# Optimization experiments

Measured on AMD Instinct MI355X. Metric: run time of the kernel, lower is better.

## Reference

```python
import jax, jax.numpy as jnp
import numpy as np

B, S, H = 2, 4096, 2048
NH, HD = 16, 128
BLOCK = 256
EPS = 1e-5


def setup_inputs() -> dict:
    key = jax.random.key(0)
    ks = jax.random.split(key, 6)
    return {
        "hidden_states": jax.random.normal(ks[0], (B, S, H), jnp.float32),
        "attention_mask": jnp.ones((B, S), jnp.float32),
        "slope_rate": jax.random.uniform(ks[1], (NH,), jnp.float32),
        "w_qkv": jax.random.normal(ks[2], (H, 3 * NH * HD), jnp.float32) * 0.02,
        "w_gate": jax.random.normal(ks[3], (H, NH * HD), jnp.float32) * 0.02,
        "w_out": jax.random.normal(ks[4], (NH * HD, H), jnp.float32) * 0.02,
        "norm_weight": jnp.ones((NH * HD,), jnp.float32),
    }


def _lightning_attention(q, k, v, slope):
    # q,k,v: [b,h,n,d]; slope: [h] positive decay rates
    b, h, n, d = q.shape
    nc = n // BLOCK
    ar = jnp.arange(BLOCK, dtype=q.dtype) + 1.0  # 1..BLOCK
    s = slope[:, None, None]  # [h,1,1]
    q_decay = jnp.exp(-s * ar[None, :, None])             # [h,BLOCK,1]
    k_decay = jnp.exp(-s * (BLOCK - ar)[None, :, None])   # [h,BLOCK,1]
    idx = ar[:, None] - ar[None, :]                        # [BLOCK,BLOCK]
    mask = (idx >= 0).astype(q.dtype)
    # mask idx before exp so masked entries don't overflow (keeps grads finite)
    diag_decay = jnp.exp(-s * (idx * mask)[None]) * mask[None]  # [h,BLOCK,BLOCK]
    block_decay = jnp.exp(-slope * BLOCK)[None, :, None, None]  # [1,h,1,1]

    def to_chunks(x):
        return x.reshape(b, h, nc, BLOCK, d).transpose(2, 0, 1, 3, 4)

    qc, kc, vc = to_chunks(q), to_chunks(k), to_chunks(v)

    def step(kv, xs):
        qi, ki, vi = xs  # [b,h,BLOCK,d]
        # inter-chunk: decayed query against carried state kv [b,h,d,d]
        o_inter = jnp.einsum("bhmd,bhde->bhme", qi * q_decay, kv)
        # intra-chunk: causal decayed attention
        attn = jnp.einsum("bhmd,bhnd->bhmn", qi, ki) * diag_decay
        o = o_inter + jnp.einsum("bhmn,bhne->bhme", attn, vi)
        kv = block_decay * kv + jnp.einsum("bhnd,bhne->bhde", ki * k_decay, vi)
        return kv, o

    kv0 = jnp.zeros((b, h, d, d), q.dtype)
    _, o = jax.lax.scan(step, kv0, (qc, kc, vc))  # o: [nc,b,h,BLOCK,d]
    return o.transpose(1, 2, 0, 3, 4).reshape(b, h, n, d)


def reference(hidden_states, attention_mask, slope_rate, w_qkv, w_gate, w_out, norm_weight):
    b, n, _ = hidden_states.shape
    qkv = jax.nn.silu(hidden_states @ w_qkv)  # act on fused qkv
    q, k, v = jnp.split(qkv, 3, axis=-1)

    def heads(x):
        return x.reshape(b, n, NH, HD).transpose(0, 2, 1, 3)

    q, k, v = heads(q), heads(k), heads(v)
    v = v * attention_mask[:, None, :, None]  # zero padded tokens
    o = _lightning_attention(q, k, v, slope_rate)  # [b,h,n,d]
    o = o.transpose(0, 2, 1, 3).reshape(b, n, NH * HD)
    # RMSNorm over head_dim*num_heads
    var = jnp.mean(o * o, axis=-1, keepdims=True)
    o = o * jax.lax.rsqrt(var + EPS) * norm_weight
    # sigmoid output gate from raw hidden_states
    o = jax.nn.sigmoid(hidden_states @ w_gate) * o
    return o @ w_out
```

## Files before the change

kernel.cpp:

```cpp
#include <hip/hip_runtime.h>
#include <cstdint>

#define B_ 2
#define S_ 4096
#define H_ 2048
#define NH_ 16
#define HD_ 128
#define BLOCK_ 256
#define NC_ (S_/BLOCK_)
#define M_ (B_*S_)
#define EPS_ 1e-5f

typedef unsigned short ushort_t;
typedef unsigned short u16x4 __attribute__((ext_vector_type(4)));
typedef short frag_ab __attribute__((ext_vector_type(8)));
typedef float frag_cd __attribute__((ext_vector_type(4)));

static __device__ inline float bf2f(ushort_t u) {
    union { unsigned int i; float f; } x;
    x.i = ((unsigned int)u) << 16;
    return x.f;
}
static __device__ inline ushort_t f2bf(float f) {
    union { float f; unsigned int i; } x;
    x.f = f;
    unsigned int r = x.i + 0x7fffu + ((x.i >> 16) & 1u);
    return (ushort_t)(r >> 16);
}

static __device__ __forceinline__ void gload_lds16(const ushort_t* g, ushort_t* l) {
    __builtin_amdgcn_global_load_lds(
        (__attribute__((address_space(1))) void*)(uintptr_t)g,
        (__attribute__((address_space(3))) void*)l,
        16, 0, 0);
}

#define FENCE_ asm volatile("" ::: "memory")
#define VMW0_  asm volatile("s_waitcnt vmcnt(0)" ::: "memory")

__global__ __launch_bounds__(256)
void cast_bf16_kernel(const float* __restrict__ in, ushort_t* __restrict__ out)
{
    int i = blockIdx.x * 256 + threadIdx.x;
    float4 v = reinterpret_cast<const float4*>(in)[i];
    u16x4 o = { f2bf(v.x), f2bf(v.y), f2bf(v.z), f2bf(v.w) };
    *reinterpret_cast<u16x4*>(&out[(size_t)i * 4]) = o;
}

__global__ __launch_bounds__(256)
void transpose_cast_kernel(const float* __restrict__ W, ushort_t* __restrict__ WT,
                           int K, int N)
{
    __shared__ float t[32][33];
    const int kb = blockIdx.y * 32, nb = blockIdx.x * 32;
    const int tx = threadIdx.x & 31, ty = threadIdx.x >> 5;
    #pragma unroll
    for (int i = 0; i < 4; ++i)
        t[ty + i * 8][tx] = W[(size_t)(kb + ty + i * 8) * N + nb + tx];
    __syncthreads();
    #pragma unroll
    for (int i = 0; i < 4; ++i)
        WT[(size_t)(nb + ty + i * 8) * K + kb + tx] = f2bf(t[tx][ty + i * 8]);
}

template<int MODE>
__global__ __launch_bounds__(256, 2)
void gemm128(const ushort_t* __restrict__ A, const ushort_t* __restrict__ BT,
             int M, int N, int K,
             float* __restrict__ Cf,
             ushort_t* __restrict__ qo, ushort_t* __restrict__ ko,
             ushort_t* __restrict__ kTo, ushort_t* __restrict__ vTo,
             ushort_t* __restrict__ gateo, const float* __restrict__ mask)
{
    __shared__ __align__(16) ushort_t LA[2][8192];
    __shared__ __align__(16) ushort_t LB[2][8192];

    const int tid  = threadIdx.x;
    const int lane = tid & 63, wid = tid >> 6;
    const int wm = wid >> 1, wn = wid & 1;
    const int l15 = lane & 15, l4 = lane >> 4;
    const int trow = tid >> 3;
    const int xk   = (tid & 7) ^ (trow & 7);

    const int nwg = gridDim.x;
    const int lin = blockIdx.x;
    const int virt = (lin & 7) * (nwg >> 3) + (lin >> 3);
    const int NBX = N >> 7;
    const int by = virt / NBX, bx = virt - by * NBX;
    const int rowBase = by * 128, colBase = bx * 128;

    frag_cd acc[4][4];
    #pragma unroll
    for (int m = 0; m < 4; ++m)
        #pragma unroll
        for (int n = 0; n < 4; ++n) acc[m][n] = 0.f;

    frag_ab fa[4][2];
    frag_ab fb[4][2];

    #define RDF(Lp, row_, sl_) \
        (*reinterpret_cast<const frag_ab*>( \
            reinterpret_cast<const char*>(Lp) + (row_) * 128 + ((((sl_) ^ ((row_) & 7)) & 7) << 4)))
    #define STG(Gp, base_, i_, kt_, Lp) \
        gload_lds16((Gp) + (size_t)((base_) + (i_) * 32 + trow) * K + (kt_) + xk * 8, \
                    (Lp) + (i_) * 2048 + wid * 512)

    const int NT = K >> 6;
    int cur = 0;
    #pragma unroll
    for (int i = 0; i < 4; ++i) { STG(A, rowBase, i, 0, LA[0]); STG(BT, colBase, i, 0, LB[0]); }
    VMW0_; FENCE_; __builtin_amdgcn_s_barrier();
    __builtin_amdgcn_sched_barrier(0);

    for (int t = 0; t < NT; ++t) {
        const ushort_t* Ab = LA[cur];
        const ushort_t* Bb = LB[cur];
        ushort_t* An = LA[cur ^ 1];
        ushort_t* Bn = LB[cur ^ 1];
        const int ktn = (t + 1) << 6;
        const bool more = (t + 1) < NT;

        if (more) {
            #pragma unroll
            for (int i = 0; i < 4; ++i) { STG(A, rowBase, i, ktn, An); STG(BT, colBase, i, ktn, Bn); }
        }

        #pragma unroll
        for (int ni = 0; ni < 4; ++ni)
            #pragma unroll
            for (int ks = 0; ks < 2; ++ks)
                fb[ni][ks] = RDF(Bb, wn * 64 + ni * 16 + l15, ks * 4 + l4);
        #pragma unroll
        for (int mi = 0; mi < 4; ++mi)
            #pragma unroll
            for (int ks = 0; ks < 2; ++ks)
                fa[mi][ks] = RDF(Ab, wm * 64 + mi * 16 + l15, ks * 4 + l4);

        __builtin_amdgcn_s_setprio(1);
        #pragma unroll
        for (int mi = 0; mi < 4; ++mi)
            #pragma unroll
            for (int ni = 0; ni < 4; ++ni)
                #pragma unroll
                for (int ks = 0; ks < 2; ++ks)
                    acc[mi][ni] = __builtin_amdgcn_mfma_f32_16x16x32_bf16(
                        fa[mi][ks], fb[ni][ks], acc[mi][ni], 0, 0, 0);
        __builtin_amdgcn_s_setprio(0);

        VMW0_; FENCE_; __builtin_amdgcn_s_barrier();
        __builtin_amdgcn_sched_barrier(0);
        cur ^= 1;
    }
    #undef RDF
    #undef STG

    const int row0 = rowBase + wm * 64;
    const int c0   = colBase + wn * 64;
    if (MODE == 0) {
        #pragma unroll
        for (int m = 0; m < 4; ++m) {
            #pragma unroll
            for (int n = 0; n < 4; ++n) {
                #pragma unroll
                for (int r = 0; r < 4; ++r) {
                    int row = row0 + m * 16 + l4 * 4 + r;
                    int col = c0 + n * 16 + l15;
                    Cf[(size_t)row * N + col] = acc[m][n][r];
                }
            }
        }
    } else {
        const int which = c0 >> 11;
        const int h     = (c0 >> 7) & 15;
        const int d0    = c0 & 127;
        const int b     = row0 >> 12;
        const int bh    = b * NH_ + h;
        #pragma unroll
        for (int m = 0; m < 4; ++m) {
            int sr0 = (row0 & 4095) + m * 16 + l4 * 4;
            #pragma unroll
            for (int n = 0; n < 4; ++n) {
                float x0 = acc[m][n][0], x1 = acc[m][n][1];
                float x2 = acc[m][n][2], x3 = acc[m][n][3];
                if (which == 3) {
                    int col_g = (c0 - 6144) + n * 16 + l15;
                    ushort_t* gp = gateo + (size_t)(row0 + m * 16 + l4 * 4) * H_ + col_g;
                    gp[0]       = f2bf(1.f / (1.f + __expf(-x0)));
                    gp[H_]      = f2bf(1.f / (1.f + __expf(-x1)));
                    gp[2 * H_]  = f2bf(1.f / (1.f + __expf(-x2)));
                    gp[3 * H_]  = f2bf(1.f / (1.f + __expf(-x3)));
                } else {
                    int d = d0 + n * 16 + l15;
                    float s0 = x0 / (1.f + __expf(-x0));
                    float s1 = x1 / (1.f + __expf(-x1));
                    float s2 = x2 / (1.f + __expf(-x2));
                    float s3 = x3 / (1.f + __expf(-x3));
                    if (which == 0) {
                        ushort_t* qp = qo + ((size_t)bh * S_ + sr0) * HD_ + d;
                        qp[0]        = f2bf(s0);
                        qp[HD_]      = f2bf(s1);
                        qp[2 * HD_]  = f2bf(s2);
                        qp[3 * HD_]  = f2bf(s3);
                    } else if (which == 1) {
                        u16x4 pk = { f2bf(s0), f2bf(s1), f2bf(s2), f2bf(s3) };
                        ushort_t* kp = ko + ((size_t)bh * S_ + sr0) * HD_ + d;
                        kp[0] = pk[0]; kp[HD_] = pk[1]; kp[2 * HD_] = pk[2]; kp[3 * HD_] = pk[3];
                        *reinterpret_cast<u16x4*>(&kTo[((size_t)bh * HD_ + d) * S_ + sr0]) = pk;
                    } else {
                        float mk0 = mask[b * S_ + sr0],     mk1 = mask[b * S_ + sr0 + 1];
                        float mk2 = mask[b * S_ + sr0 + 2], mk3 = mask[b * S_ + sr0 + 3];
                        u16x4 pk = { f2bf(s0 * mk0), f2bf(s1 * mk1), f2bf(s2 * mk2), f2bf(s3 * mk3) };
                        *reinterpret_cast<u16x4*>(&vTo[((size_t)bh * HD_ + d) * S_ + sr0]) = pk;
                    }
                }
            }
        }
    }
}

__global__ __launch_bounds__(256)
void kv_chunk_mfma(const ushort_t* __restrict__ kT, const ushort_t* __restrict__ vT,
                   const float* __restrict__ slope, ushort_t* __restrict__ kvT)
{
    const int c = blockIdx.x, bh = blockIdx.y;
    const float s = slope[bh & 15];
    const int tid = threadIdx.x, lane = tid & 63, w = tid >> 6;
    const int l15 = lane & 15, l4 = lane >> 4;
    __shared__ float dec[BLOCK_];
    __shared__ __align__(16) ushort_t VTl[128 * 64];
    __shared__ __align__(16) ushort_t KTl[128 * 64];
    dec[tid] = __expf(-s * (float)(BLOCK_ - 1 - tid));

    frag_cd acc[2][8];
    #pragma unroll
    for (int mf = 0; mf < 2; ++mf)
        #pragma unroll
        for (int df = 0; df < 8; ++df) acc[mf][df] = 0.f;

    for (int nt = 0; nt < 4; ++nt) {
        __syncthreads();
        #pragma unroll
        for (int i = 0; i < 4; ++i) {
            int u = tid + i * 256;
            int row = u >> 3, slot = u & 7;
            size_t gsrc = ((size_t)bh * HD_ + row) * S_ + c * BLOCK_ + nt * 64 + slot * 8;
            frag_ab v8 = *reinterpret_cast<const frag_ab*>(vT + gsrc);
            *reinterpret_cast<frag_ab*>((char*)VTl + row * 128 + ((slot * 16) ^ ((row & 7) << 4))) = v8;
            frag_ab k8 = *reinterpret_cast<const frag_ab*>(kT + gsrc);
            frag_ab kd;
            #pragma unroll
            for (int j = 0; j < 8; ++j)
                kd[j] = (short)f2bf(bf2f((ushort_t)k8[j]) * dec[nt * 64 + slot * 8 + j]);
            *reinterpret_cast<frag_ab*>((char*)KTl + row * 128 + ((slot * 16) ^ ((row & 7) << 4))) = kd;
        }
        __syncthreads();
        #pragma unroll
        for (int ks = 0; ks < 2; ++ks) {
            frag_ab a[2];
            #pragma unroll
            for (int mf = 0; mf < 2; ++mf)
                a[mf] = *reinterpret_cast<const frag_ab*>(
                    (char*)VTl + (w * 32 + mf * 16 + l15) * 128 + ((ks * 64 + l4 * 16) ^ ((l15 & 7) << 4)));
            #pragma unroll
            for (int df = 0; df < 8; ++df) {
                frag_ab bk = *reinterpret_cast<const frag_ab*>(
                    (char*)KTl + (df * 16 + l15) * 128 + ((ks * 64 + l4 * 16) ^ ((l15 & 7) << 4)));
                acc[0][df] = __builtin_amdgcn_mfma_f32_16x16x32_bf16(a[0], bk, acc[0][df], 0, 0, 0);
                acc[1][df] = __builtin_amdgcn_mfma_f32_16x16x32_bf16(a[1], bk, acc[1][df], 0, 0, 0);
            }
        }
    }
    ushort_t* out = kvT + ((size_t)bh * NC_ + c) * 16384;
    #pragma unroll
    for (int mf = 0; mf < 2; ++mf)
        #pragma unroll
        for (int df = 0; df < 8; ++df)
            #pragma unroll
            for (int r = 0; r < 4; ++r) {
                int e = w * 32 + mf * 16 + l4 * 4 + r;
                int d = df * 16 + l15;
                out[e * 128 + d] = f2bf(acc[mf][df][r]);
            }
}

__global__ __launch_bounds__(256)
void kv_scan_kernel(const float* __restrict__ slope, const ushort_t* __restrict__ kvT,
                    ushort_t* __restrict__ sT)
{
    const int es = blockIdx.x, bh = blockIdx.y;
    const float s = slope[bh & 15];
    const float bd = __expf(-s * (float)BLOCK_);
    const int tid = threadIdx.x;
    float st[16];
    #pragma unroll
    for (int i = 0; i < 16; ++i) st[i] = 0.f;
    for (int c = 0; c < NC_; ++c) {
        const ushort_t* p = kvT + ((size_t)bh * NC_ + c) * 16384;
        ushort_t* qp = sT + ((size_t)bh * NC_ + c) * 16384;
        #pragma unroll
        for (int i = 0; i < 16; ++i) {
            int lin = tid + i * 256;
            int off = (lin >> 5) * 128 + es * 32 + (lin & 31);
            float x = bf2f(p[off]);
            qp[off] = f2bf(st[i]);
            st[i] = bd * st[i] + x;
        }
    }
}

__global__ __launch_bounds__(512)
void attn_mfma(const ushort_t* __restrict__ q, const ushort_t* __restrict__ k,
               const ushort_t* __restrict__ vT, const ushort_t* __restrict__ sT,
               const float* __restrict__ slope, float* __restrict__ o)
{
    const int c = blockIdx.x, bh = blockIdx.y;
    const int h = bh & 15, b = bh >> 4;
    const float s = slope[h];
    const int tid = threadIdx.x, lane = tid & 63, w = tid >> 6;
    const int l15 = lane & 15, l4 = lane >> 4;

    __shared__ __align__(16) ushort_t SH[16384];
    __shared__ __align__(16) ushort_t P[8][2048];

    frag_ab aq[2][4];
    #pragma unroll
    for (int mf = 0; mf < 2; ++mf)
        #pragma unroll
        for (int ks = 0; ks < 4; ++ks) {
            int row = c * BLOCK_ + w * 32 + mf * 16 + l15;
            aq[mf][ks] = *reinterpret_cast<const frag_ab*>(
                q + ((size_t)bh * S_ + row) * HD_ + ks * 32 + l4 * 8);
        }

    frag_cd oa[2][8];
    #pragma unroll
    for (int mf = 0; mf < 2; ++mf)
        #pragma unroll
        for (int ef = 0; ef < 8; ++ef) oa[mf][ef] = 0.f;

    const int wrow = w * 32;
    for (int nt = 0; nt < 4; ++nt) {
        __syncthreads();
        #pragma unroll
        for (int i = 0; i < 2; ++i) {
            int u = tid + i * 512;
            int n = u >> 4, slot = u & 15;
            frag_ab k8 = *reinterpret_cast<const frag_ab*>(
                k + ((size_t)bh * S_ + c * BLOCK_ + nt * 64 + n) * HD_ + slot * 8);
            *reinterpret_cast<frag_ab*>((char*)SH + n * 256 + ((slot * 16) ^ ((n & 7) << 4))) = k8;
        }
        #pragma unroll
        for (int i = 0; i < 2; ++i) {
            int u = tid + i * 512;
            int e = u >> 3, slot = u & 7;
            frag_ab v8 = *reinterpret_cast<const frag_ab*>(
                vT + ((size_t)bh * HD_ + e) * S_ + c * BLOCK_ + nt * 64 + slot * 8);
            *reinterpret_cast<frag_ab*>((char*)SH + 16384 + e * 128 + ((slot * 16) ^ ((e & 7) << 4))) = v8;
        }
        __syncthreads();
        if (nt * 64 > wrow + 31) continue;

        frag_cd pacc[2][4];
        #pragma unroll
        for (int mf = 0; mf < 2; ++mf)
            #pragma unroll
            for (int nf = 0; nf < 4; ++nf) pacc[mf][nf] = 0.f;
        #pragma unroll
        for (int ks = 0; ks < 4; ++ks)
            #pragma unroll
            for (int nf = 0; nf < 4; ++nf) {
                frag_ab bk = *reinterpret_cast<const frag_ab*>(
                    (char*)SH + (nf * 16 + l15) * 256 + ((ks * 64 + l4 * 16) ^ ((l15 & 7) << 4)));
                pacc[0][nf] = __builtin_amdgcn_mfma_f32_16x16x32_bf16(aq[0][ks], bk, pacc[0][nf], 0, 0, 0);
                pacc[1][nf] = __builtin_amdgcn_mfma_f32_16x16x32_bf16(aq[1][ks], bk, pacc[1][nf], 0, 0, 0);
            }
        #pragma unroll
        for (int mf = 0; mf < 2; ++mf)
            #pragma unroll
            for (int nf = 0; nf < 4; ++nf)
                #pragma unroll
                for (int r = 0; r < 4; ++r) {
                    int m = mf * 16 + l4 * 4 + r;
                    int mrow = wrow + m;
                    int ncol = nt * 64 + nf * 16 + l15;
                    float pv = 0.f;
                    if (mrow >= ncol) pv = pacc[mf][nf][r] * __expf(s * (float)(ncol - mrow));
                    *reinterpret_cast<ushort_t*>(
                        (char*)&P[w][0] + m * 128 + (((nf * 16 + l15) * 2) ^ ((m & 7) << 4))) = f2bf(pv);
                }
        __builtin_amdgcn_sched_barrier(0);
        #pragma unroll
        for (int ks = 0; ks < 2; ++ks) {
            frag_ab ap[2];
            #pragma unroll
            for (int mf = 0; mf < 2; ++mf)
                ap[mf] = *reinterpret_cast<const frag_ab*>(
                    (char*)&P[w][0] + (mf * 16 + l15) * 128 + ((ks * 64 + l4 * 16) ^ ((l15 & 7) << 4)));
            #pragma unroll
            for (int ef = 0; ef < 8; ++ef) {
                frag_ab bv = *reinterpret_cast<const frag_ab*>(
                    (char*)SH + 16384 + (ef * 16 + l15) * 128 + ((ks * 64 + l4 * 16) ^ ((l15 & 7) << 4)));
                oa[0][ef] = __builtin_amdgcn_mfma_f32_16x16x32_bf16(ap[0], bv, oa[0][ef], 0, 0, 0);
                oa[1][ef] = __builtin_amdgcn_mfma_f32_16x16x32_bf16(ap[1], bv, oa[1][ef], 0, 0, 0);
            }
        }
    }

    __syncthreads();
    #pragma unroll
    for (int i = 0; i < 4; ++i) {
        int u = tid + i * 512;
        int e = u >> 4, slot = u & 15;
        frag_ab s8 = *reinterpret_cast<const frag_ab*>(
            sT + ((size_t)(bh * NC_ + c)) * 16384 + e * 128 + slot * 8);
        *reinterpret_cast<frag_ab*>((char*)SH + e * 256 + ((slot * 16) ^ ((e & 7) << 4))) = s8;
    }
    __syncthreads();
    #pragma unroll
    for (int mf = 0; mf < 2; ++mf) {
        float qd = __expf(-s * (float)(wrow + mf * 16 + l15 + 1));
        #pragma unroll
        for (int ks = 0; ks < 4; ++ks) {
            frag_ab v = aq[mf][ks];
            #pragma unroll
            for (int j = 0; j < 8; ++j)
                v[j] = (short)f2bf(bf2f((ushort_t)v[j]) * qd);
            aq[mf][ks] = v;
        }
    }
    #pragma unroll
    for (int ks = 0; ks < 4; ++ks)
        #pragma unroll
        for (int ef = 0; ef < 8; ++ef) {
            frag_ab bs = *reinterpret_cast<const frag_ab*>(
                (char*)SH + (ef * 16 + l15) * 256 + ((ks * 64 + l4 * 16) ^ ((l15 & 7) << 4)));
            oa[0][ef] = __builtin_amdgcn_mfma_f32_16x16x32_bf16(aq[0][ks], bs, oa[0][ef], 0, 0, 0);
            oa[1][ef] = __builtin_amdgcn_mfma_f32_16x16x32_bf16(aq[1][ks], bs, oa[1][ef], 0, 0, 0);
        }
    #pragma unroll
    for (int mf = 0; mf < 2; ++mf)
        #pragma unroll
        for (int ef = 0; ef < 8; ++ef)
            #pragma unroll
            for (int r = 0; r < 4; ++r) {
                int row = c * BLOCK_ + wrow + mf * 16 + l4 * 4 + r;
                int col = h * HD_ + ef * 16 + l15;
                o[((size_t)(b * S_ + row)) * H_ + col] = oa[mf][ef][r];
            }
}

__global__ __launch_bounds__(256)
void norm_gate_kernel(const float* __restrict__ o, const ushort_t* __restrict__ gate,
                      const float* __restrict__ nw, ushort_t* __restrict__ on)
{
    const int row = blockIdx.x;
    const int tid = threadIdx.x;
    const float* orow = o + (size_t)row * H_;
    const ushort_t* grow = gate + (size_t)row * H_;
    ushort_t* onrow = on + (size_t)row * H_;
    float vals[8];
    float ss = 0.f;
    #pragma unroll
    for (int i = 0; i < 8; ++i) {
        vals[i] = orow[tid + i * 256];
        ss += vals[i] * vals[i];
    }
    __shared__ float red[256];
    red[tid] = ss;
    __syncthreads();
    #pragma unroll
    for (int st = 128; st > 0; st >>= 1) {
        if (tid < st) red[tid] += red[tid + st];
        __syncthreads();
    }
    float scale = rsqrtf(red[0] * (1.f / (float)H_) + EPS_);
    #pragma unroll
    for (int i = 0; i < 8; ++i) {
        int cidx = tid + i * 256;
        onrow[cidx] = f2bf(vals[i] * scale * nw[cidx] * bf2f(grow[cidx]));
    }
}

extern "C" void kernel_launch(void* const* d_in, const int* in_sizes, int n_in,
                              void* d_out, int out_size, void* d_ws, size_t ws_size,
                              hipStream_t stream)
{
    const float* hidden = (const float*)d_in[0];
    const float* mask   = (const float*)d_in[1];
    const float* slope  = (const float*)d_in[2];
    const float* w_qkv  = (const float*)d_in[3];
    const float* w_gate = (const float*)d_in[4];
    const float* w_out  = (const float*)d_in[5];
    const float* nw     = (const float*)d_in[6];

    const size_t MH = (size_t)M_ * H_;
    ushort_t* hid_bf  = (ushort_t*)d_ws;
    ushort_t* on_ws   = hid_bf;
    ushort_t* wqkvT   = hid_bf + MH;
    ushort_t* wgateT  = wqkvT + (size_t)6144 * 2048;
    ushort_t* kvT_ws  = wqkvT;
    ushort_t* sT_ws   = wqkvT + MH / 2;
    ushort_t* woutT   = wqkvT;
    ushort_t* q_ws    = hid_bf + 2 * MH;
    ushort_t* k_ws    = q_ws + MH;
    ushort_t* vT_ws   = k_ws + MH;
    ushort_t* gate_ws = vT_ws + MH;
    ushort_t* kT_ws   = (ushort_t*)d_out;
    float*    o_f32   = (float*)d_out;

    dim3 blk(256);
    cast_bf16_kernel<<<(MH / 4) / 256, blk, 0, stream>>>(hidden, hid_bf);
    transpose_cast_kernel<<<dim3(6144 / 32, 2048 / 32), blk, 0, stream>>>(w_qkv, wqkvT, 2048, 6144);
    transpose_cast_kernel<<<dim3(2048 / 32, 2048 / 32), blk, 0, stream>>>(w_gate, wgateT, 2048, 2048);
    gemm128<2><<<dim3((M_ / 128) * (8192 / 128)), blk, 0, stream>>>(
        hid_bf, wqkvT, M_, 8192, 2048,
        nullptr, q_ws, k_ws, kT_ws, vT_ws, gate_ws, mask);
    kv_chunk_mfma<<<dim3(NC_, B_ * NH_), blk, 0, stream>>>(kT_ws, vT_ws, slope, kvT_ws);
    kv_scan_kernel<<<dim3(4, B_ * NH_), blk, 0, stream>>>(slope, kvT_ws, sT_ws);
    attn_mfma<<<dim3(NC_, B_ * NH_), dim3(512), 0, stream>>>(
        q_ws, k_ws, vT_ws, sT_ws, slope, o_f32);
    transpose_cast_kernel<<<dim3(2048 / 32, 2048 / 32), blk, 0, stream>>>(w_out, woutT, 2048, 2048);
    norm_gate_kernel<<<M_, blk, 0, stream>>>(o_f32, gate_ws, nw, on_ws);
    gemm128<0><<<dim3((M_ / 128) * (2048 / 128)), blk, 0, stream>>>(
        on_ws, woutT, M_, 2048, 2048,
        (float*)d_out, nullptr, nullptr, nullptr, nullptr, nullptr, nullptr);
}
```

Before: 591.8 us.

## Use 256x256 tile, 8-wave GEMM with interleaved prefetch for fused QKV/gate projection

Replaces the 128x128, 4-wave GEMM for the large QKV+gate projection with a 256x256 tile, 512-thread kernel. Each wave computes a 128x64 sub-tile. Global-to-LDS prefetches for the next K tile are split into chunks interleaved between MFMA groups, with partial vmcnt waits instead of a full drain. The aim is more data reuse per LDS load and better overlap of memory traffic with compute. The cost is 128KB of LDS per block, more accumulator registers, fewer blocks in the grid, and a delicate wait-count ordering that must stay correct. The output GEMM keeps the old 128 kernel, now specialised.

```diff
diff --git a/kernel.cpp b/kernel.cpp
--- a/kernel.cpp
+++ b/kernel.cpp
@@ -36,6 +36,8 @@
 }
 
 #define FENCE_ asm volatile("" ::: "memory")
+#define VMW8_  asm volatile("s_waitcnt vmcnt(8)" ::: "memory")
+#define VMW2_  asm volatile("s_waitcnt vmcnt(2)" ::: "memory")
 #define VMW0_  asm volatile("s_waitcnt vmcnt(0)" ::: "memory")
 
 __global__ __launch_bounds__(256)
@@ -64,20 +66,20 @@
 }
 
 template<int MODE>
-__global__ __launch_bounds__(256, 2)
-void gemm128(const ushort_t* __restrict__ A, const ushort_t* __restrict__ BT,
+__global__ __launch_bounds__(512, 2)
+void gemm256(const ushort_t* __restrict__ A, const ushort_t* __restrict__ BT,
              int M, int N, int K,
              float* __restrict__ Cf,
              ushort_t* __restrict__ qo, ushort_t* __restrict__ ko,
              ushort_t* __restrict__ kTo, ushort_t* __restrict__ vTo,
              ushort_t* __restrict__ gateo, const float* __restrict__ mask)
 {
-    __shared__ __align__(16) ushort_t LA[2][8192];
-    __shared__ __align__(16) ushort_t LB[2][8192];
+    __shared__ __align__(16) ushort_t LA[2][16384];
+    __shared__ __align__(16) ushort_t LB[2][16384];
 
     const int tid  = threadIdx.x;
     const int lane = tid & 63, wid = tid >> 6;
-    const int wm = wid >> 1, wn = wid & 1;
+    const int wm = wid >> 2, wn = wid & 3;
     const int l15 = lane & 15, l4 = lane >> 4;
     const int trow = tid >> 3;
     const int xk   = (tid & 7) ^ (trow & 7);
@@ -85,112 +87,152 @@
     const int nwg = gridDim.x;
     const int lin = blockIdx.x;
     const int virt = (lin & 7) * (nwg >> 3) + (lin >> 3);
-    const int NBX = N >> 7;
+    const int NBX = N >> 8;
     const int by = virt / NBX, bx = virt - by * NBX;
-    const int rowBase = by * 128, colBase = bx * 128;
-
-    frag_cd acc[4][4];
-    #pragma unroll
-    for (int m = 0; m < 4; ++m)
+    const int rowBase = by * 256, colBase = bx * 256;
+
+    frag_cd acc[8][4];
+    #pragma unroll
+    for (int m = 0; m < 8; ++m)
         #pragma unroll
         for (int n = 0; n < 4; ++n) acc[m][n] = 0.f;
 
     frag_ab fa[4][2];
-    frag_ab fb[4][2];
+    frag_ab fb[2][2][2];
 
     #define RDF(Lp, row_, sl_) \
         (*reinterpret_cast<const frag_ab*>( \
             reinterpret_cast<const char*>(Lp) + (row_) * 128 + ((((sl_) ^ ((row_) & 7)) & 7) << 4)))
     #define STG(Gp, base_, i_, kt_, Lp) \
-        gload_lds16((Gp) + (size_t)((base_) + (i_) * 32 + trow) * K + (kt_) + xk * 8, \
-                    (Lp) + (i_) * 2048 + wid * 512)
+        gload_lds16((Gp) + (size_t)((base_) + (i_) * 64 + trow) * K + (kt_) + xk * 8, \
+                    (Lp) + (i_) * 4096 + wid * 512)
 
     const int NT = K >> 6;
-    int cur = 0;
-    #pragma unroll
-    for (int i = 0; i < 4; ++i) { STG(A, rowBase, i, 0, LA[0]); STG(BT, colBase, i, 0, LB[0]); }
-    VMW0_; FENCE_; __builtin_amdgcn_s_barrier();
+
+    #define KTILE(AbP, BbP, AnP, BnP, TNEXT)                                        \
+    do {                                                                            \
+        const bool more = (TNEXT) < NT;                                             \
+        const int ktn = (TNEXT) << 6;                                               \
+                                                                            \
+        _Pragma("unroll")                                                           \
+        for (int mi = 0; mi < 4; ++mi)                                              \
+            _Pragma("unroll")                                                       \
+            for (int ks = 0; ks < 2; ++ks)                                          \
+                fa[mi][ks] = RDF(AbP, wm * 128 + mi * 16 + l15, ks * 4 + l4);       \
+        _Pragma("unroll")                                                           \
+        for (int ni = 0; ni < 2; ++ni)                                              \
+            _Pragma("unroll")                                                       \
+            for (int ks = 0; ks < 2; ++ks)                                          \
+                fb[0][ni][ks] = RDF(BbP, wn * 64 + ni * 16 + l15, ks * 4 + l4);     \
+        if (more) { STG(BT, colBase, 0, ktn, BnP); STG(BT, colBase, 1, ktn, BnP); } \
+        __builtin_amdgcn_s_setprio(1);                                              \
+        _Pragma("unroll")                                                           \
+        for (int mi = 0; mi < 4; ++mi)                                              \
+            _Pragma("unroll")                                                       \
+            for (int ni = 0; ni < 2; ++ni)                                          \
+                _Pragma("unroll")                                                   \
+                for (int ks = 0; ks < 2; ++ks)                                      \
+                    acc[mi][ni] = __builtin_amdgcn_mfma_f32_16x16x32_bf16(          \
+                        fa[mi][ks], fb[0][ni][ks], acc[mi][ni], 0, 0, 0);           \
+        __builtin_amdgcn_s_setprio(0);                                              \
+                                                                            \
+        _Pragma("unroll")                                                           \
+        for (int ni = 0; ni < 2; ++ni)                                              \
+            _Pragma("unroll")                                                       \
+            for (int ks = 0; ks < 2; ++ks)                                          \
+                fb[1][ni][ks] = RDF(BbP, wn * 64 + 32 + ni * 16 + l15, ks * 4 + l4);\
+        if (more) { STG(BT, colBase, 2, ktn, BnP); STG(BT, colBase, 3, ktn, BnP); } \
+        __builtin_amdgcn_s_setprio(1);                                              \
+        _Pragma("unroll")                                                           \
+        for (int mi = 0; mi < 4; ++mi)                                              \
+            _Pragma("unroll")                                                       \
+            for (int ni = 0; ni < 2; ++ni)                                          \
+                _Pragma("unroll")                                                   \
+                for (int ks = 0; ks < 2; ++ks)                                      \
+                    acc[mi][2 + ni] = __builtin_amdgcn_mfma_f32_16x16x32_bf16(      \
+                        fa[mi][ks], fb[1][ni][ks], acc[mi][2 + ni], 0, 0, 0);       \
+        __builtin_amdgcn_s_setprio(0);                                              \
+        if (more) { VMW8_; } else { VMW0_; }                                        \
+        FENCE_; __builtin_amdgcn_s_barrier();                                       \
+        __builtin_amdgcn_sched_barrier(0);                                          \
+                                                                            \
+        _Pragma("unroll")                                                           \
+        for (int mi = 0; mi < 4; ++mi)                                              \
+            _Pragma("unroll")                                                       \
+            for (int ks = 0; ks < 2; ++ks)                                          \
+                fa[mi][ks] = RDF(AbP, wm * 128 + 64 + mi * 16 + l15, ks * 4 + l4);  \
+        if (more) { STG(A, rowBase, 0, ktn, AnP); STG(A, rowBase, 2, ktn, AnP); }   \
+        __builtin_amdgcn_s_setprio(1);                                              \
+        _Pragma("unroll")                                                           \
+        for (int mi = 0; mi < 4; ++mi)                                              \
+            _Pragma("unroll")                                                       \
+            for (int ni = 0; ni < 2; ++ni)                                          \
+                _Pragma("unroll")                                                   \
+                for (int ks = 0; ks < 2; ++ks)                                      \
+                    acc[4 + mi][ni] = __builtin_amdgcn_mfma_f32_16x16x32_bf16(      \
+                        fa[mi][ks], fb[0][ni][ks], acc[4 + mi][ni], 0, 0, 0);       \
+        __builtin_amdgcn_s_setprio(0);                                              \
+                                                                            \
+        if (more) { STG(A, rowBase, 1, ktn, AnP); STG(A, rowBase, 3, ktn, AnP); }   \
+        __builtin_amdgcn_s_setprio(1);                                              \
+        _Pragma("unroll")                                                           \
+        for (int mi = 0; mi < 4; ++mi)                                              \
+            _Pragma("unroll")                                                       \
+            for (int ni = 0; ni < 2; ++ni)                                          \
+                _Pragma("unroll")                                                   \
+                for (int ks = 0; ks < 2; ++ks)                                      \
+                    acc[4 + mi][2 + ni] = __builtin_amdgcn_mfma_f32_16x16x32_bf16(  \
+                        fa[mi][ks], fb[1][ni][ks], acc[4 + mi][2 + ni], 0, 0, 0);   \
+        __builtin_amdgcn_s_setprio(0);                                              \
+        if (more) { VMW2_; }                                                        \
+        FENCE_; __builtin_amdgcn_s_barrier();                                       \
+        __builtin_amdgcn_sched_barrier(0);                                          \
+    } while (0)
+
+    STG(BT, colBase, 0, 0, &LB[0][0]); STG(BT, colBase, 1, 0, &LB[0][0]);
+    STG(BT, colBase, 2, 0, &LB[0][0]); STG(BT, colBase, 3, 0, &LB[0][0]);
+    STG(A,  rowBase, 0, 0, &LA[0][0]); STG(A,  rowBase, 2, 0, &LA[0][0]);
+    STG(A,  rowBase, 1, 0, &LA[0][0]); STG(A,  rowBase, 3, 0, &LA[0][0]);
+    VMW2_; FENCE_; __builtin_amdgcn_s_barrier();
     __builtin_amdgcn_sched_barrier(0);
 
-    for (int t = 0; t < NT; ++t) {
-        const ushort_t* Ab = LA[cur];
-        const ushort_t* Bb = LB[cur];
-        ushort_t* An = LA[cur ^ 1];
-        ushort_t* Bn = LB[cur ^ 1];
-        const int ktn = (t + 1) << 6;
-        const bool more = (t + 1) < NT;
-
-        if (more) {
-            #pragma unroll
-            for (int i = 0; i < 4; ++i) { STG(A, rowBase, i, ktn, An); STG(BT, colBase, i, ktn, Bn); }
-        }
-
-        #pragma unroll
-        for (int ni = 0; ni < 4; ++ni)
-            #pragma unroll
-            for (int ks = 0; ks < 2; ++ks)
-                fb[ni][ks] = RDF(Bb, wn * 64 + ni * 16 + l15, ks * 4 + l4);
-        #pragma unroll
-        for (int mi = 0; mi < 4; ++mi)
-            #pragma unroll
-            for (int ks = 0; ks < 2; ++ks)
-                fa[mi][ks] = RDF(Ab, wm * 64 + mi * 16 + l15, ks * 4 + l4);
-
-        __builtin_amdgcn_s_setprio(1);
-        #pragma unroll
-        for (int mi = 0; mi < 4; ++mi)
-            #pragma unroll
-            for (int ni = 0; ni < 4; ++ni)
-                #pragma unroll
-                for (int ks = 0; ks < 2; ++ks)
-                    acc[mi][ni] = __builtin_amdgcn_mfma_f32_16x16x32_bf16(
-                        fa[mi][ks], fb[ni][ks], acc[mi][ni], 0, 0, 0);
-        __builtin_amdgcn_s_setprio(0);
-
-        VMW0_; FENCE_; __builtin_amdgcn_s_barrier();
-        __builtin_amdgcn_sched_barrier(0);
-        cur ^= 1;
-    }
+    for (int t2 = 0; t2 < NT; t2 += 2) {
+        KTILE(&LA[0][0], &LB[0][0], &LA[1][0], &LB[1][0], t2 + 1);
+        KTILE(&LA[1][0], &LB[1][0], &LA[0][0], &LB[0][0], t2 + 2);
+    }
+    #undef KTILE
     #undef RDF
     #undef STG
 
-    const int row0 = rowBase + wm * 64;
+    const int row0 = rowBase + wm * 128;
     const int c0   = colBase + wn * 64;
-    if (MODE == 0) {
-        #pragma unroll
-        for (int m = 0; m < 4; ++m) {
-            #pragma unroll
-            for (int n = 0; n < 4; ++n) {
-                #pragma unroll
-                for (int r = 0; r < 4; ++r) {
-                    int row = row0 + m * 16 + l4 * 4 + r;
-                    int col = c0 + n * 16 + l15;
-                    Cf[(size_t)row * N + col] = acc[m][n][r];
-                }
-            }
-        }
-    } else {
+    {
         const int which = c0 >> 11;
         const int h     = (c0 >> 7) & 15;
         const int d0    = c0 & 127;
         const int b     = row0 >> 12;
         const int bh    = b * NH_ + h;
         #pragma unroll
-        for (int m = 0; m < 4; ++m) {
-            int sr0 = (row0 & 4095) + m * 16 + l4 * 4;
+        for (int m = 0; m < 8; ++m) {
+            int mr = (m >> 2) * 64 + (m & 3) * 16;
+            int sr0 = (row0 & 4095) + mr + l4 * 4;
             #pragma unroll
             for (int n = 0; n < 4; ++n) {
+                int nc = (n >> 1) * 32 + (n & 1) * 16;
                 float x0 = acc[m][n][0], x1 = acc[m][n][1];
                 float x2 = acc[m][n][2], x3 = acc[m][n][3];
-                if (which == 3) {
-                    int col_g = (c0 - 6144) + n * 16 + l15;
-                    ushort_t* gp = gateo + (size_t)(row0 + m * 16 + l4 * 4) * H_ + col_g;
+                if (MODE == 0) {
+                    float* cp = Cf + (size_t)(row0 + mr + l4 * 4) * N + c0 + nc + l15;
+                    cp[0] = x0; cp[N] = x1; cp[2 * (size_t)N] = x2; cp[3 * (size_t)N] = x3;
+                } else if (which == 3) {
+                    int col_g = (c0 - 6144) + nc + l15;
+                    ushort_t* gp = gateo + (size_t)(row0 + mr + l4 * 4) * H_ + col_g;
                     gp[0]       = f2bf(1.f / (1.f + __expf(-x0)));
                     gp[H_]      = f2bf(1.f / (1.f + __expf(-x1)));
                     gp[2 * H_]  = f2bf(1.f / (1.f + __expf(-x2)));
                     gp[3 * H_]  = f2bf(1.f / (1.f + __expf(-x3)));
                 } else {
-                    int d = d0 + n * 16 + l15;
+                    int d = d0 + nc + l15;
                     float s0 = x0 / (1.f + __expf(-x0));
                     float s1 = x1 / (1.f + __expf(-x1));
                     float s2 = x2 / (1.f + __expf(-x2));
@@ -218,6 +260,106 @@
     }
 }
 
+__global__ __launch_bounds__(256, 2)
+void gemm128(const ushort_t* __restrict__ A, const ushort_t* __restrict__ BT,
+             int M, int N, int K, float* __restrict__ Cf)
+{
+    __shared__ __align__(16) ushort_t LA[2][8192];
+    __shared__ __align__(16) ushort_t LB[2][8192];
+
+    const int tid  = threadIdx.x;
+    const int lane = tid & 63, wid = tid >> 6;
+    const int wm = wid >> 1, wn = wid & 1;
+    const int l15 = lane & 15, l4 = lane >> 4;
+    const int trow = tid >> 3;
+    const int xk   = (tid & 7) ^ (trow & 7);
+
+    const int nwg = gridDim.x;
+    const int lin = blockIdx.x;
+    const int virt = (lin & 7) * (nwg >> 3) + (lin >> 3);
+    const int NBX = N >> 7;
+    const int by = virt / NBX, bx = virt - by * NBX;
+    const int rowBase = by * 128, colBase = bx * 128;
+
+    frag_cd acc[4][4];
+    #pragma unroll
+    for (int m = 0; m < 4; ++m)
+        #pragma unroll
+        for (int n = 0; n < 4; ++n) acc[m][n] = 0.f;
+
+    frag_ab fa[4][2];
+    frag_ab fb[4][2];
+
+    #define RDF(Lp, row_, sl_) \
+        (*reinterpret_cast<const frag_ab*>( \
+            reinterpret_cast<const char*>(Lp) + (row_) * 128 + ((((sl_) ^ ((row_) & 7)) & 7) << 4)))
+    #define STG(Gp, base_, i_, kt_, Lp) \
+        gload_lds16((Gp) + (size_t)((base_) + (i_) * 32 + trow) * K + (kt_) + xk * 8, \
+                    (Lp) + (i_) * 2048 + wid * 512)
+
+    const int NT = K >> 6;
+    int cur = 0;
+    #pragma unroll
+    for (int i = 0; i < 4; ++i) { STG(A, rowBase, i, 0, LA[0]); STG(BT, colBase, i, 0, LB[0]); }
+    VMW0_; FENCE_; __builtin_amdgcn_s_barrier();
+    __builtin_amdgcn_sched_barrier(0);
+
+    for (int t = 0; t < NT; ++t) {
+        const ushort_t* Ab = LA[cur];
+        const ushort_t* Bb = LB[cur];
+        ushort_t* An = LA[cur ^ 1];
+        ushort_t* Bn = LB[cur ^ 1];
+        const int ktn = (t + 1) << 6;
+        const bool more = (t + 1) < NT;
+
+        if (more) {
+            #pragma unroll
+            for (int i = 0; i < 4; ++i) { STG(A, rowBase, i, ktn, An); STG(BT, colBase, i, ktn, Bn); }
+        }
+
+        #pragma unroll
+        for (int ni = 0; ni < 4; ++ni)
+            #pragma unroll
+            for (int ks = 0; ks < 2; ++ks)
+                fb[ni][ks] = RDF(Bb, wn * 64 + ni * 16 + l15, ks * 4 + l4);
+        #pragma unroll
+        for (int mi = 0; mi < 4; ++mi)
+            #pragma unroll
+            for (int ks = 0; ks < 2; ++ks)
+                fa[mi][ks] = RDF(Ab, wm * 64 + mi * 16 + l15, ks * 4 + l4);
+
+        __builtin_amdgcn_s_setprio(1);
+        #pragma unroll
+        for (int mi = 0; mi < 4; ++mi)
+            #pragma unroll
+            for (int ni = 0; ni < 4; ++ni)
+                #pragma unroll
+                for (int ks = 0; ks < 2; ++ks)
+                    acc[mi][ni] = __builtin_amdgcn_mfma_f32_16x16x32_bf16(
+                        fa[mi][ks], fb[ni][ks], acc[mi][ni], 0, 0, 0);
+        __builtin_amdgcn_s_setprio(0);
+
+        VMW0_; FENCE_; __builtin_amdgcn_s_barrier();
+        __builtin_amdgcn_sched_barrier(0);
+        cur ^= 1;
+    }
+    #undef RDF
+    #undef STG
+
+    const int row0 = rowBase + wm * 64;
+    const int c0   = colBase + wn * 64;
+    #pragma unroll
+    for (int m = 0; m < 4; ++m)
+        #pragma unroll
+        for (int n = 0; n < 4; ++n)
+            #pragma unroll
+            for (int r = 0; r < 4; ++r) {
+                int row = row0 + m * 16 + l4 * 4 + r;
+                int col = c0 + n * 16 + l15;
+                Cf[(size_t)row * N + col] = acc[m][n][r];
+            }
+}
+
 __global__ __launch_bounds__(256)
 void kv_chunk_mfma(const ushort_t* __restrict__ kT, const ushort_t* __restrict__ vT,
                    const float* __restrict__ slope, ushort_t* __restrict__ kvT)
@@ -512,7 +654,7 @@
     cast_bf16_kernel<<<(MH / 4) / 256, blk, 0, stream>>>(hidden, hid_bf);
     transpose_cast_kernel<<<dim3(6144 / 32, 2048 / 32), blk, 0, stream>>>(w_qkv, wqkvT, 2048, 6144);
     transpose_cast_kernel<<<dim3(2048 / 32, 2048 / 32), blk, 0, stream>>>(w_gate, wgateT, 2048, 2048);
-    gemm128<2><<<dim3((M_ / 128) * (8192 / 128)), blk, 0, stream>>>(
+    gemm256<2><<<dim3((M_ / 256) * (8192 / 256)), dim3(512), 0, stream>>>(
         hid_bf, wqkvT, M_, 8192, 2048,
         nullptr, q_ws, k_ws, kT_ws, vT_ws, gate_ws, mask);
     kv_chunk_mfma<<<dim3(NC_, B_ * NH_), blk, 0, stream>>>(kT_ws, vT_ws, slope, kvT_ws);
@@ -521,7 +663,6 @@
         q_ws, k_ws, vT_ws, sT_ws, slope, o_f32);
     transpose_cast_kernel<<<dim3(2048 / 32, 2048 / 32), blk, 0, stream>>>(w_out, woutT, 2048, 2048);
     norm_gate_kernel<<<M_, blk, 0, stream>>>(o_f32, gate_ws, nw, on_ws);
-    gemm128<0><<<dim3((M_ / 128) * (2048 / 128)), blk, 0, stream>>>(
-        on_ws, woutT, M_, 2048, 2048,
-        (float*)d_out, nullptr, nullptr, nullptr, nullptr, nullptr, nullptr);
-}
+    gemm128<<<dim3((M_ / 128) * (2048 / 128)), blk, 0, stream>>>(
+        on_ws, woutT, M_, 2048, 2048, (float*)d_out);
+}
```

Result: faster. 562.2 us (-5.0%).
